# Optimization experiments

Hardware: AMD Instinct MI355X
Metric: run time of the kernel (lower is better)

## Reference

```python
import jax, jax.numpy as jnp
import numpy as np

ENTITY_ID_COL = 0  # EntityState 'id' attribute column
NUM_NPC_TYPES = 5
LN_EPS = 1e-5
NEG = -1e9


def layernorm(x, g, b):
    m = jnp.mean(x, axis=-1, keepdims=True)
    v = jnp.mean((x - m) ** 2, axis=-1, keepdims=True)
    return (x - m) * jax.lax.rsqrt(v + LN_EPS) * g + b


def gat_layer(x, mask, W, a_src, a_dst, ln_g, ln_b, num_heads, concat):
    B, N, _ = x.shape
    D = a_src.shape[-1]
    h = jnp.matmul(x, W).reshape(B, N, num_heads, D)          # [B,N,H,D]
    e_i = jnp.sum(h * a_src, axis=-1)                          # [B,N,H]
    e_j = jnp.sum(h * a_dst, axis=-1)                          # [B,N,H]
    # additive attention: e[b,i,j,h] = leakyrelu(e_i[b,i,h] + e_j[b,j,h])
    e = jax.nn.leaky_relu(e_i[:, :, None, :] + e_j[:, None, :, :], 0.2)
    mm = mask[:, :, None, None] * mask[:, None, :, None]       # [B,N,N,1]
    e = jnp.where(mm == 0, NEG, e)
    attn = jax.nn.softmax(e, axis=2)                           # softmax over j
    h_prime = jnp.einsum('bnjh,bjhd->bnhd', attn, h)
    if concat:
        h_prime = h_prime.reshape(B, N, num_heads * D)
    else:
        h_prime = h_prime.mean(axis=2)
    if h_prime.shape[-1] == x.shape[-1]:
        h_prime = layernorm(h_prime + x, ln_g, ln_b)
    else:
        h_prime = layernorm(h_prime, ln_g, ln_b)
    return h_prime


def setup_inputs() -> dict:
    key = jax.random.key(0)
    ks = jax.random.split(key, 12)
    B, N = 8, 1024
    entity_dim, hidden, heads, input_size = 31, 256, 4, 256
    d_head = hidden // heads  # 64
    merged_dim = entity_dim + 4  # 35 (npc_type expanded to 5 one-hot cols)

    agents = jax.random.normal(ks[0], (B, N, entity_dim), dtype=jnp.float32)
    npc_type = jax.random.randint(ks[1], (B, N), 0, NUM_NPC_TYPES).astype(jnp.float32)
    valid = (jax.random.uniform(ks[2], (B, N)) < 0.9).astype(jnp.float32)
    ids = jnp.arange(1, N + 1, dtype=jnp.float32)[None, :] * valid
    ids = ids.at[:, 0].set(1.0)  # guarantee id 1 exists in every batch row
    agents = agents.at[:, :, 0].set(ids)
    agents = agents.at[:, :, 1].set(npc_type)
    my_id = jnp.ones((B,), dtype=jnp.int32)

    def xavier(k, shape, fan_in, fan_out, gain=1.414):
        bound = gain * np.sqrt(6.0 / (fan_in + fan_out))
        return jax.random.uniform(k, shape, jnp.float32, -bound, bound)

    Wp = xavier(ks[3], (merged_dim, hidden), merged_dim, hidden, 1.0)
    bp = jnp.zeros((hidden,), jnp.float32)
    W1 = xavier(ks[4], (hidden, heads * d_head), hidden, heads * d_head)
    a_src1 = xavier(ks[5], (heads, d_head), heads, d_head)
    a_dst1 = xavier(ks[6], (heads, d_head), heads, d_head)
    ln1_g = jnp.ones((heads * d_head,), jnp.float32)
    ln1_b = jnp.zeros((heads * d_head,), jnp.float32)
    W2 = xavier(ks[7], (hidden, heads * d_head), hidden, heads * d_head)
    a_src2 = xavier(ks[8], (heads, d_head), heads, d_head)
    a_dst2 = xavier(ks[9], (heads, d_head), heads, d_head)
    ln2_g = jnp.ones((d_head,), jnp.float32)
    ln2_b = jnp.zeros((d_head,), jnp.float32)
    Wa = xavier(ks[10], (d_head, hidden), d_head, hidden, 1.0)
    ba = jnp.zeros((hidden,), jnp.float32)
    Wm = xavier(ks[11], (d_head, input_size), d_head, input_size, 1.0)
    bm = jnp.zeros((input_size,), jnp.float32)
    return dict(agents=agents, my_id=my_id, Wp=Wp, bp=bp,
                W1=W1, a_src1=a_src1, a_dst1=a_dst1, ln1_g=ln1_g, ln1_b=ln1_b,
                W2=W2, a_src2=a_src2, a_dst2=a_dst2, ln2_g=ln2_g, ln2_b=ln2_b,
                Wa=Wa, ba=ba, Wm=Wm, bm=bm)


def reference(agents, my_id, Wp, bp, W1, a_src1, a_dst1, ln1_g, ln1_b,
              W2, a_src2, a_dst2, ln2_g, ln2_b, Wa, ba, Wm, bm):
    num_heads = a_src1.shape[0]
    npc_type = agents[:, :, 1].astype(jnp.int32)
    one_hot = jax.nn.one_hot(npc_type, NUM_NPC_TYPES, dtype=jnp.float32)
    merged = jnp.concatenate([agents[:, :, :1], one_hot, agents[:, :, 2:]], axis=-1)
    mask = (merged[:, :, ENTITY_ID_COL] != 0).astype(jnp.float32)   # [B,N]
    proj = jnp.matmul(merged, Wp) + bp                              # [B,N,hidden]
    h1 = jax.nn.relu(gat_layer(proj, mask, W1, a_src1, a_dst1, ln1_g, ln1_b, num_heads, True))
    h2 = jax.nn.relu(gat_layer(h1, mask, W2, a_src2, a_dst2, ln2_g, ln2_b, num_heads, False))
    agent_embeddings = jnp.matmul(h2, Wa) + ba                      # [B,N,hidden]
    self_mask = merged[:, :, ENTITY_ID_COL] == my_id[:, None].astype(jnp.float32)
    idx = jnp.argmax(self_mask.astype(jnp.int32), axis=1)           # [B]
    my_emb = h2[jnp.arange(h2.shape[0]), idx]                       # [B,d_head]
    my_emb = jax.nn.relu(jnp.matmul(my_emb, Wm) + bm)
    return (agent_embeddings, my_emb)
```

## Files before the change

### kernel.cpp

```cpp
#include <hip/hip_runtime.h>
#include <hip/hip_bf16.h>

typedef _Float16 f16x8 __attribute__((ext_vector_type(8)));
typedef float f32x4 __attribute__((ext_vector_type(4)));

__global__ __launch_bounds__(256) void k_proj(
    const float* __restrict__ agents, const int* __restrict__ my_id,
    const float* __restrict__ Wp, const float* __restrict__ bp,
    float* __restrict__ proj, float* __restrict__ mask, int* __restrict__ idx)
{
  int blk = blockIdx.x;
  int b = blk >> 10, n = blk & 1023;
  __shared__ float arow[32];
  int t = threadIdx.x;
  if (t < 31) arow[t] = agents[((size_t)(b * 1024 + n)) * 31 + t];
  __syncthreads();
  float id = arow[0];
  int npc = (int)arow[1];
  float acc = bp[t] + id * Wp[t] + Wp[(1 + npc) * 256 + t];
#pragma unroll
  for (int c = 2; c < 31; ++c) acc += arow[c] * Wp[(4 + c) * 256 + t];
  proj[((size_t)(b * 1024 + n)) * 256 + t] = acc;
  if (t == 0) {
    mask[b * 1024 + n] = (id != 0.f) ? 1.f : 0.f;
    if (id == (float)my_id[b]) atomicMin(&idx[b], n);
  }
}

__global__ __launch_bounds__(256) void k_gemm(
    const float* __restrict__ A, const float* __restrict__ B,
    const float* __restrict__ bias, float* __restrict__ C, int K)
{
  __shared__ float As[64][68];
  __shared__ float Bs[64][68];
  int tid = threadIdx.x;
  int bi = blockIdx.x >> 2, bj = blockIdx.x & 3;
  int i0 = bi << 6, j0 = bj << 6;
  int ti4 = (tid & 15) << 2, tj4 = (tid >> 4) << 2;
  int r = tid >> 2, c0 = (tid & 3) << 4;
  float acc[4][4];
#pragma unroll
  for (int a = 0; a < 4; ++a)
#pragma unroll
    for (int q = 0; q < 4; ++q) acc[a][q] = 0.f;

  for (int k0 = 0; k0 < K; k0 += 64) {
    const float4* Ap4 = (const float4*)(A + (size_t)(i0 + r) * K + k0 + c0);
    float4 aa0 = Ap4[0], aa1 = Ap4[1], aa2 = Ap4[2], aa3 = Ap4[3];
    As[c0 + 0][r] = aa0.x; As[c0 + 1][r] = aa0.y; As[c0 + 2][r] = aa0.z; As[c0 + 3][r] = aa0.w;
    As[c0 + 4][r] = aa1.x; As[c0 + 5][r] = aa1.y; As[c0 + 6][r] = aa1.z; As[c0 + 7][r] = aa1.w;
    As[c0 + 8][r] = aa2.x; As[c0 + 9][r] = aa2.y; As[c0 +10][r] = aa2.z; As[c0 +11][r] = aa2.w;
    As[c0 +12][r] = aa3.x; As[c0 +13][r] = aa3.y; As[c0 +14][r] = aa3.z; As[c0 +15][r] = aa3.w;
    const float4* Bp4 = (const float4*)(B + (size_t)(k0 + r) * 256 + j0 + c0);
    float4 bb0 = Bp4[0], bb1 = Bp4[1], bb2 = Bp4[2], bb3 = Bp4[3];
    *(float4*)&Bs[r][c0 + 0]  = bb0;
    *(float4*)&Bs[r][c0 + 4]  = bb1;
    *(float4*)&Bs[r][c0 + 8]  = bb2;
    *(float4*)&Bs[r][c0 + 12] = bb3;
    __syncthreads();
#pragma unroll
    for (int k = 0; k < 64; ++k) {
      float4 av = *(const float4*)&As[k][ti4];
      float4 bv = *(const float4*)&Bs[k][tj4];
      acc[0][0] += av.x * bv.x; acc[0][1] += av.x * bv.y; acc[0][2] += av.x * bv.z; acc[0][3] += av.x * bv.w;
      acc[1][0] += av.y * bv.x; acc[1][1] += av.y * bv.y; acc[1][2] += av.y * bv.z; acc[1][3] += av.y * bv.w;
      acc[2][0] += av.z * bv.x; acc[2][1] += av.z * bv.y; acc[2][2] += av.z * bv.z; acc[2][3] += av.z * bv.w;
      acc[3][0] += av.w * bv.x; acc[3][1] += av.w * bv.y; acc[3][2] += av.w * bv.z; acc[3][3] += av.w * bv.w;
    }
    __syncthreads();
  }
  float4 bb;
  if (bias) bb = *(const float4*)&bias[j0 + tj4];
  else { bb.x = bb.y = bb.z = bb.w = 0.f; }
#pragma unroll
  for (int ii = 0; ii < 4; ++ii) {
    float4 o;
    o.x = acc[ii][0] + bb.x; o.y = acc[ii][1] + bb.y;
    o.z = acc[ii][2] + bb.z; o.w = acc[ii][3] + bb.w;
    *(float4*)&C[(size_t)(i0 + ti4 + ii) * 256 + j0 + tj4] = o;
  }
}

__global__ __launch_bounds__(256) void k_edges(
    const float* __restrict__ h, const float* __restrict__ a_src,
    const float* __restrict__ a_dst, float* __restrict__ esrc, float* __restrict__ edst)
{
  __shared__ float as_[256], ad_[256];
  int t = threadIdx.x;
  as_[t] = a_src[t];
  ad_[t] = a_dst[t];
  __syncthreads();
  int w = t >> 6, l = t & 63;
  int row = blockIdx.x * 4 + w;
  const float* x = h + (size_t)row * 256;
  float ps[4], pd[4];
#pragma unroll
  for (int hh = 0; hh < 4; ++hh) {
    float v = x[hh * 64 + l];
    ps[hh] = v * as_[hh * 64 + l];
    pd[hh] = v * ad_[hh * 64 + l];
  }
#pragma unroll
  for (int hh = 0; hh < 4; ++hh) {
    for (int o = 32; o; o >>= 1) {
      ps[hh] += __shfl_down(ps[hh], o);
      pd[hh] += __shfl_down(pd[hh], o);
    }
  }
  if (l == 0) {
    int b = row >> 10, n = row & 1023;
#pragma unroll
    for (int hh = 0; hh < 4; ++hh) {
      esrc[((b * 4 + hh) << 10) + n] = ps[hh];
      edst[((b * 4 + hh) << 10) + n] = pd[hh];
    }
  }
}

__global__ __launch_bounds__(256) void k_emax(
    const float* __restrict__ edst, const float* __restrict__ mask, float* __restrict__ Mmax)
{
  int bh = blockIdx.x;
  int b = bh >> 2;
  int t = threadIdx.x;
  float v = -1e30f;
  for (int j = t; j < 1024; j += 256)
    if (mask[(b << 10) + j] != 0.f) v = fmaxf(v, edst[(bh << 10) + j]);
  for (int o = 32; o; o >>= 1) v = fmaxf(v, __shfl_down(v, o));
  __shared__ float red[4];
  if ((t & 63) == 0) red[t >> 6] = v;
  __syncthreads();
  if (t == 0) Mmax[bh] = fmaxf(fmaxf(red[0], red[1]), fmaxf(red[2], red[3]));
}

__global__ __launch_bounds__(256) void k_prep(
    const float* __restrict__ h, _Float16* __restrict__ hT)
{
  int blk = blockIdx.x;
  int c = blk & 31, hh = (blk >> 5) & 3, b = blk >> 7;
  int t = threadIdx.x;
  __shared__ _Float16 tile[32][72];
  {
    int jr = t >> 3, dg = t & 7;
    const float* src = h + ((size_t)(b * 1024 + c * 32 + jr)) * 256 + hh * 64 + dg * 8;
    float4 a = *(const float4*)src;
    float4 b4 = *(const float4*)(src + 4);
    _Float16* tp = &tile[jr][dg * 8];
    tp[0] = (_Float16)a.x;  tp[1] = (_Float16)a.y;  tp[2] = (_Float16)a.z;  tp[3] = (_Float16)a.w;
    tp[4] = (_Float16)b4.x; tp[5] = (_Float16)b4.y; tp[6] = (_Float16)b4.z; tp[7] = (_Float16)b4.w;
  }
  __syncthreads();
  {
    int d = t >> 2, q = t & 3;
    _Float16 o[8];
#pragma unroll
    for (int s = 0; s < 8; ++s) o[s] = tile[q * 8 + s][d];
    _Float16* dst = hT + ((size_t)((b * 4 + hh) * 32 + c)) * 2048 + d * 32 + q * 8;
    *(uint4*)dst = *(const uint4*)o;
  }
}

template <int LAYER>
__global__ __launch_bounds__(256) void k_attn_mfma(
    const _Float16* __restrict__ hT, const float* __restrict__ esrc,
    const float* __restrict__ edst, const float* __restrict__ Mmax,
    const float* __restrict__ mask, const float* __restrict__ resid,
    const float* __restrict__ g, const float* __restrict__ be,
    float* __restrict__ out)
{
  __shared__ __align__(16) char smem[40960];
  __shared__ float esrcL[16][4], mL[16][4];
  __shared__ float maskL[16], MhL[4];
  __shared__ float sInvS[4][16];
  __shared__ float statM[16], statR[16];

  int t = threadIdx.x;
  int hID = t >> 6, l = t & 63;
  int b = blockIdx.x & 7;
  int it = blockIdx.x >> 3;
  int i0 = it << 4;

  if (t < 16) maskL[t] = mask[(b << 10) + i0 + t];
  if (t < 4) MhL[t] = Mmax[(b << 2) + t];
  if (t < 64) {
    int ii = t >> 2, hh = t & 3;
    esrcL[ii][hh] = esrc[(((b << 2) + hh) << 10) + i0 + ii];
  }
  __syncthreads();
  if (t < 64) {
    int ii = t >> 2, hh = t & 3;
    float m = 0.f;
    if (maskL[ii] != 0.f) {
      float v = esrcL[ii][hh] + MhL[hh];
      m = v > 0.f ? v : 0.2f * v;
    }
    mL[ii][hh] = m;
  }
  __syncthreads();

  int iloc = l & 15;
  float esr = esrcL[iloc][hID];
  float mr = mL[iloc][hID];
  float mskI = maskL[iloc];
  int jg = (l >> 4) << 3;

  const float* ej_base = edst + (((b << 2) + hID) << 10);
  const float* mk_base = mask + (b << 10);
  const char* gT = (const char*)hT + ((size_t)((b * 4 + hID) * 32)) * 4096;
  char* hb = smem + hID * 10240;

  f32x4 C0 = {0.f,0.f,0.f,0.f}, C1 = C0, C2 = C0, C3 = C0;
  float sp = 0.f;

  {
    const uint4* gs = (const uint4*)(gT + l * 64);
    uint4 s0 = gs[0], s1 = gs[1], s2 = gs[2], s3 = gs[3];
    uint4* wp = (uint4*)(hb + l * 80);
    wp[0] = s0; wp[1] = s1; wp[2] = s2; wp[3] = s3;
  }
  int cur = 0;

  for (int c = 0; c < 32; ++c) {
    uint4 n0, n1, n2, n3;
    if (c < 31) {
      const uint4* gs = (const uint4*)(gT + (size_t)(c + 1) * 4096 + l * 64);
      n0 = gs[0]; n1 = gs[1]; n2 = gs[2]; n3 = gs[3];
    }
    int j0 = c << 5;
    float4 e0 = *(const float4*)(ej_base + j0 + jg);
    float4 e1 = *(const float4*)(ej_base + j0 + jg + 4);
    float4 m0 = *(const float4*)(mk_base + j0 + jg);
    float4 m1 = *(const float4*)(mk_base + j0 + jg + 4);
    float w[8];
    float ev[8] = {e0.x, e0.y, e0.z, e0.w, e1.x, e1.y, e1.z, e1.w};
    float mv[8] = {m0.x, m0.y, m0.z, m0.w, m1.x, m1.y, m1.z, m1.w};
    if (mskI != 0.f) {
#pragma unroll
      for (int q = 0; q < 8; ++q) {
        float v = esr + ev[q];
        v = v > 0.f ? v : 0.2f * v;
        w[q] = (mv[q] != 0.f) ? __expf(v - mr) : 0.f;
      }
    } else {
#pragma unroll
      for (int q = 0; q < 8; ++q) w[q] = 1.f;
    }
    f16x8 af;
#pragma unroll
    for (int q = 0; q < 8; ++q) { sp += w[q]; af[q] = (_Float16)w[q]; }
    const char* rp = hb + cur * 5120 + (l & 15) * 80 + (l >> 4) * 16;
    f16x8 b0 = *(const f16x8*)(rp);
    f16x8 b1 = *(const f16x8*)(rp + 1280);
    f16x8 b2 = *(const f16x8*)(rp + 2560);
    f16x8 b3 = *(const f16x8*)(rp + 3840);
    C0 = __builtin_amdgcn_mfma_f32_16x16x32_f16(af, b0, C0, 0, 0, 0);
    C1 = __builtin_amdgcn_mfma_f32_16x16x32_f16(af, b1, C1, 0, 0, 0);
    C2 = __builtin_amdgcn_mfma_f32_16x16x32_f16(af, b2, C2, 0, 0, 0);
    C3 = __builtin_amdgcn_mfma_f32_16x16x32_f16(af, b3, C3, 0, 0, 0);
    if (c < 31) {
      uint4* wp = (uint4*)(hb + (cur ^ 1) * 5120 + l * 80);
      wp[0] = n0; wp[1] = n1; wp[2] = n2; wp[3] = n3;
      cur ^= 1;
    }
  }

  sp += __shfl_xor(sp, 16);
  sp += __shfl_xor(sp, 32);
  if (l < 16) sInvS[hID][l] = 1.f / sp;
  __syncthreads();

  float (*y)[256] = (float (*)[256])smem;
  {
    int rbase = (l >> 4) << 2;
    int col = (hID << 6) + (l & 15);
#pragma unroll
    for (int r = 0; r < 4; ++r) {
      float sv = sInvS[hID][rbase + r];
      y[rbase + r][col +  0] = C0[r] * sv;
      y[rbase + r][col + 16] = C1[r] * sv;
      y[rbase + r][col + 32] = C2[r] * sv;
      y[rbase + r][col + 48] = C3[r] * sv;
    }
  }
  __syncthreads();

  if (LAYER == 1) {
#pragma unroll
    for (int i = 0; i < 16; ++i)
      y[i][t] += resid[((size_t)(b * 1024 + i0 + i)) * 256 + t];
    __syncthreads();
#pragma unroll
    for (int rr = 0; rr < 4; ++rr) {
      int i = (hID << 2) + rr;
      float v0 = y[i][l], v1 = y[i][64 + l], v2 = y[i][128 + l], v3 = y[i][192 + l];
      float s = v0 + v1 + v2 + v3;
      float q = v0 * v0 + v1 * v1 + v2 * v2 + v3 * v3;
      for (int o = 32; o; o >>= 1) { s += __shfl_xor(s, o); q += __shfl_xor(q, o); }
      if (l == 0) {
        float mean = s * (1.f / 256.f);
        float var = q * (1.f / 256.f) - mean * mean;
        statM[i] = mean;
        statR[i] = rsqrtf(var + 1e-5f);
      }
    }
    __syncthreads();
#pragma unroll
    for (int i = 0; i < 16; ++i) {
      float yv = y[i][t];
      float o_ = (yv - statM[i]) * statR[i] * g[t] + be[t];
      out[((size_t)(b * 1024 + i0 + i)) * 256 + t] = fmaxf(o_, 0.f);
    }
  } else {
#pragma unroll
    for (int rr = 0; rr < 4; ++rr) {
      int i = (hID << 2) + rr;
      float v = 0.25f * (y[i][l] + y[i][64 + l] + y[i][128 + l] + y[i][192 + l]);
      float s = v, q = v * v;
      for (int o = 32; o; o >>= 1) { s += __shfl_xor(s, o); q += __shfl_xor(q, o); }
      float mean = s * (1.f / 64.f);
      float var = q * (1.f / 64.f) - mean * mean;
      float rstd = rsqrtf(var + 1e-5f);
      float o_ = (v - mean) * rstd * g[l] + be[l];
      out[((size_t)(b * 1024 + i0 + i)) * 64 + l] = fmaxf(o_, 0.f);
    }
  }
}

__global__ __launch_bounds__(256) void k_myemb(
    const float* __restrict__ h2, const int* __restrict__ idx,
    const float* __restrict__ Wm, const float* __restrict__ bm, float* __restrict__ out)
{
  __shared__ float row[64];
  int t = threadIdx.x;
  for (int b = 0; b < 8; ++b) {
    int n = idx[b];
    if (t < 64) row[t] = h2[((size_t)(b * 1024 + n)) * 64 + t];
    __syncthreads();
    float acc = bm[t];
#pragma unroll
    for (int d = 0; d < 64; ++d) acc += row[d] * Wm[d * 256 + t];
    out[2097152 + b * 256 + t] = fmaxf(acc, 0.f);
    __syncthreads();
  }
}

extern "C" void kernel_launch(void* const* d_in, const int* in_sizes, int n_in,
                              void* d_out, int out_size, void* d_ws, size_t ws_size,
                              hipStream_t stream) {
  const float* agents = (const float*)d_in[0];
  const int* my_id = (const int*)d_in[1];
  const float* Wp = (const float*)d_in[2];
  const float* bp = (const float*)d_in[3];
  const float* W1 = (const float*)d_in[4];
  const float* a_src1 = (const float*)d_in[5];
  const float* a_dst1 = (const float*)d_in[6];
  const float* ln1_g = (const float*)d_in[7];
  const float* ln1_b = (const float*)d_in[8];
  const float* W2 = (const float*)d_in[9];
  const float* a_src2 = (const float*)d_in[10];
  const float* a_dst2 = (const float*)d_in[11];
  const float* ln2_g = (const float*)d_in[12];
  const float* ln2_b = (const float*)d_in[13];
  const float* Wa = (const float*)d_in[14];
  const float* ba = (const float*)d_in[15];
  const float* Wm = (const float*)d_in[16];
  const float* bm = (const float*)d_in[17];
  float* out = (float*)d_out;

  float* W = (float*)d_ws;
  float* mask = W;
  float* Mmax = W + 8192;
  int* idx = (int*)(W + 8224);
  float* esrc = W + 16384;
  float* edst = W + 49152;
  float* proj = W + 81920;
  float* htmp = W + 2179072;
  float* h1 = W + 4276224;
  float* h2 = W + 6373376;
  _Float16* hT = (_Float16*)(W + 6897664);

  hipMemsetAsync(idx, 0x7F, 8 * sizeof(int), stream);
  k_proj<<<8192, 256, 0, stream>>>(agents, my_id, Wp, bp, proj, mask, idx);

  k_gemm<<<512, 256, 0, stream>>>(proj, W1, nullptr, htmp, 256);
  k_prep<<<1024, 256, 0, stream>>>(htmp, hT);
  k_edges<<<2048, 256, 0, stream>>>(htmp, a_src1, a_dst1, esrc, edst);
  k_emax<<<32, 256, 0, stream>>>(edst, mask, Mmax);
  k_attn_mfma<1><<<512, 256, 0, stream>>>(hT, esrc, edst, Mmax, mask, proj, ln1_g, ln1_b, h1);

  k_gemm<<<512, 256, 0, stream>>>(h1, W2, nullptr, htmp, 256);
  k_prep<<<1024, 256, 0, stream>>>(htmp, hT);
  k_edges<<<2048, 256, 0, stream>>>(htmp, a_src2, a_dst2, esrc, edst);
  k_emax<<<32, 256, 0, stream>>>(edst, mask, Mmax);
  k_attn_mfma<2><<<512, 256, 0, stream>>>(hT, esrc, edst, Mmax, mask, nullptr, ln2_g, ln2_b, h2);

  k_gemm<<<512, 256, 0, stream>>>(h2, Wa, ba, out, 64);
  k_myemb<<<1, 256, 0, stream>>>(h2, idx, Wm, bm, out);
}
```

Measured before the change: 243.1 us.

## Replace FP32 SIMT GEMMs with split-fp16 MFMA GEMMs using pre-transposed weights

Swaps the scalar FP32 tiled GEMM for an MFMA 16x16x32 f16 kernel. Each fp32 operand is split into hi and lo halves, and three MFMAs per tile keep accuracy close to fp32. Weights are transposed each call by a small k_wt kernel so B tiles load contiguously along K. This trades scalar FMA throughput for matrix-core throughput, at the cost of extra conversion work, three extra launches, and more syncs per K step with a smaller 32-wide K tile.

Measured after the change: 235.8 us. 1.03x faster.

```diff
diff --git a/kernel.cpp b/kernel.cpp
--- a/kernel.cpp
+++ b/kernel.cpp
@@ -27,57 +27,116 @@
   }
 }
 
-__global__ __launch_bounds__(256) void k_gemm(
-    const float* __restrict__ A, const float* __restrict__ B,
-    const float* __restrict__ bias, float* __restrict__ C, int K)
-{
-  __shared__ float As[64][68];
-  __shared__ float Bs[64][68];
-  int tid = threadIdx.x;
+__global__ __launch_bounds__(256) void k_wt(
+    const float* __restrict__ W, float* __restrict__ Wt, int K)
+{
+  __shared__ float tl[32][33];
+  int bk = blockIdx.x >> 3, bj = blockIdx.x & 7;
+  int tc = threadIdx.x & 31, tr = threadIdx.x >> 5;
+#pragma unroll
+  for (int r = 0; r < 4; ++r) {
+    int row = tr * 4 + r;
+    tl[row][tc] = W[(size_t)(bk * 32 + row) * 256 + bj * 32 + tc];
+  }
+  __syncthreads();
+#pragma unroll
+  for (int r = 0; r < 4; ++r) {
+    int row = tr * 4 + r;
+    Wt[(size_t)(bj * 32 + row) * K + bk * 32 + tc] = tl[tc][row];
+  }
+}
+
+template <int K>
+__global__ __launch_bounds__(256) void k_gemm_mfma(
+    const float* __restrict__ A, const float* __restrict__ BtF,
+    const float* __restrict__ bias, float* __restrict__ C)
+{
+  __shared__ __align__(16) _Float16 AsH[64 * 40], AsL[64 * 40];
+  __shared__ __align__(16) _Float16 BsH[64 * 40], BsL[64 * 40];
+  int t = threadIdx.x;
+  int w = t >> 6, l = t & 63;
   int bi = blockIdx.x >> 2, bj = blockIdx.x & 3;
   int i0 = bi << 6, j0 = bj << 6;
-  int ti4 = (tid & 15) << 2, tj4 = (tid >> 4) << 2;
-  int r = tid >> 2, c0 = (tid & 3) << 4;
-  float acc[4][4];
-#pragma unroll
-  for (int a = 0; a < 4; ++a)
-#pragma unroll
-    for (int q = 0; q < 4; ++q) acc[a][q] = 0.f;
-
-  for (int k0 = 0; k0 < K; k0 += 64) {
-    const float4* Ap4 = (const float4*)(A + (size_t)(i0 + r) * K + k0 + c0);
-    float4 aa0 = Ap4[0], aa1 = Ap4[1], aa2 = Ap4[2], aa3 = Ap4[3];
-    As[c0 + 0][r] = aa0.x; As[c0 + 1][r] = aa0.y; As[c0 + 2][r] = aa0.z; As[c0 + 3][r] = aa0.w;
-    As[c0 + 4][r] = aa1.x; As[c0 + 5][r] = aa1.y; As[c0 + 6][r] = aa1.z; As[c0 + 7][r] = aa1.w;
-    As[c0 + 8][r] = aa2.x; As[c0 + 9][r] = aa2.y; As[c0 +10][r] = aa2.z; As[c0 +11][r] = aa2.w;
-    As[c0 +12][r] = aa3.x; As[c0 +13][r] = aa3.y; As[c0 +14][r] = aa3.z; As[c0 +15][r] = aa3.w;
-    const float4* Bp4 = (const float4*)(B + (size_t)(k0 + r) * 256 + j0 + c0);
-    float4 bb0 = Bp4[0], bb1 = Bp4[1], bb2 = Bp4[2], bb3 = Bp4[3];
-    *(float4*)&Bs[r][c0 + 0]  = bb0;
-    *(float4*)&Bs[r][c0 + 4]  = bb1;
-    *(float4*)&Bs[r][c0 + 8]  = bb2;
-    *(float4*)&Bs[r][c0 + 12] = bb3;
-    __syncthreads();
-#pragma unroll
-    for (int k = 0; k < 64; ++k) {
-      float4 av = *(const float4*)&As[k][ti4];
-      float4 bv = *(const float4*)&Bs[k][tj4];
-      acc[0][0] += av.x * bv.x; acc[0][1] += av.x * bv.y; acc[0][2] += av.x * bv.z; acc[0][3] += av.x * bv.w;
-      acc[1][0] += av.y * bv.x; acc[1][1] += av.y * bv.y; acc[1][2] += av.y * bv.z; acc[1][3] += av.y * bv.w;
-      acc[2][0] += av.z * bv.x; acc[2][1] += av.z * bv.y; acc[2][2] += av.z * bv.z; acc[2][3] += av.z * bv.w;
-      acc[3][0] += av.w * bv.x; acc[3][1] += av.w * bv.y; acc[3][2] += av.w * bv.z; acc[3][3] += av.w * bv.w;
-    }
-    __syncthreads();
-  }
-  float4 bb;
-  if (bias) bb = *(const float4*)&bias[j0 + tj4];
-  else { bb.x = bb.y = bb.z = bb.w = 0.f; }
-#pragma unroll
-  for (int ii = 0; ii < 4; ++ii) {
-    float4 o;
-    o.x = acc[ii][0] + bb.x; o.y = acc[ii][1] + bb.y;
-    o.z = acc[ii][2] + bb.z; o.w = acc[ii][3] + bb.w;
-    *(float4*)&C[(size_t)(i0 + ti4 + ii) * 256 + j0 + tj4] = o;
+  int srow = t >> 2, skq = (t & 3) << 3;
+
+  f32x4 C0 = {0.f, 0.f, 0.f, 0.f}, C1 = C0, C2 = C0, C3 = C0;
+
+  for (int k0 = 0; k0 < K; k0 += 32) {
+    {
+      const float* ap = A + (size_t)(i0 + srow) * K + k0 + skq;
+      float4 a0 = *(const float4*)ap, a1 = *(const float4*)(ap + 4);
+      float av[8] = {a0.x, a0.y, a0.z, a0.w, a1.x, a1.y, a1.z, a1.w};
+      _Float16 hi[8], lo[8];
+#pragma unroll
+      for (int q = 0; q < 8; ++q) {
+        hi[q] = (_Float16)av[q];
+        lo[q] = (_Float16)(av[q] - (float)hi[q]);
+      }
+      *(uint4*)&AsH[srow * 40 + skq] = *(const uint4*)hi;
+      *(uint4*)&AsL[srow * 40 + skq] = *(const uint4*)lo;
+    }
+    {
+      const float* bp = BtF + (size_t)(j0 + srow) * K + k0 + skq;
+      float4 b0 = *(const float4*)bp, b1 = *(const float4*)(bp + 4);
+      float bv[8] = {b0.x, b0.y, b0.z, b0.w, b1.x, b1.y, b1.z, b1.w};
+      _Float16 hi[8], lo[8];
+#pragma unroll
+      for (int q = 0; q < 8; ++q) {
+        hi[q] = (_Float16)bv[q];
+        lo[q] = (_Float16)(bv[q] - (float)hi[q]);
+      }
+      *(uint4*)&BsH[srow * 40 + skq] = *(const uint4*)hi;
+      *(uint4*)&BsL[srow * 40 + skq] = *(const uint4*)lo;
+    }
+    __syncthreads();
+    int fr = l & 15;
+    int fk = (l >> 4) << 3;
+    f16x8 ah = *(const f16x8*)&AsH[(w * 16 + fr) * 40 + fk];
+    f16x8 al = *(const f16x8*)&AsL[(w * 16 + fr) * 40 + fk];
+    {
+      f16x8 bh = *(const f16x8*)&BsH[(0 * 16 + fr) * 40 + fk];
+      f16x8 bl = *(const f16x8*)&BsL[(0 * 16 + fr) * 40 + fk];
+      C0 = __builtin_amdgcn_mfma_f32_16x16x32_f16(ah, bh, C0, 0, 0, 0);
+      C0 = __builtin_amdgcn_mfma_f32_16x16x32_f16(ah, bl, C0, 0, 0, 0);
+      C0 = __builtin_amdgcn_mfma_f32_16x16x32_f16(al, bh, C0, 0, 0, 0);
+    }
+    {
+      f16x8 bh = *(const f16x8*)&BsH[(1 * 16 + fr) * 40 + fk];
+      f16x8 bl = *(const f16x8*)&BsL[(1 * 16 + fr) * 40 + fk];
+      C1 = __builtin_amdgcn_mfma_f32_16x16x32_f16(ah, bh, C1, 0, 0, 0);
+      C1 = __builtin_amdgcn_mfma_f32_16x16x32_f16(ah, bl, C1, 0, 0, 0);
+      C1 = __builtin_amdgcn_mfma_f32_16x16x32_f16(al, bh, C1, 0, 0, 0);
+    }
+    {
+      f16x8 bh = *(const f16x8*)&BsH[(2 * 16 + fr) * 40 + fk];
+      f16x8 bl = *(const f16x8*)&BsL[(2 * 16 + fr) * 40 + fk];
+      C2 = __builtin_amdgcn_mfma_f32_16x16x32_f16(ah, bh, C2, 0, 0, 0);
+      C2 = __builtin_amdgcn_mfma_f32_16x16x32_f16(ah, bl, C2, 0, 0, 0);
+      C2 = __builtin_amdgcn_mfma_f32_16x16x32_f16(al, bh, C2, 0, 0, 0);
+    }
+    {
+      f16x8 bh = *(const f16x8*)&BsH[(3 * 16 + fr) * 40 + fk];
+      f16x8 bl = *(const f16x8*)&BsL[(3 * 16 + fr) * 40 + fk];
+      C3 = __builtin_amdgcn_mfma_f32_16x16x32_f16(ah, bh, C3, 0, 0, 0);
+      C3 = __builtin_amdgcn_mfma_f32_16x16x32_f16(ah, bl, C3, 0, 0, 0);
+      C3 = __builtin_amdgcn_mfma_f32_16x16x32_f16(al, bh, C3, 0, 0, 0);
+    }
+    __syncthreads();
+  }
+
+  int rbase = i0 + w * 16 + ((l >> 4) << 2);
+  int cb = j0 + (l & 15);
+  float b0 = bias ? bias[cb] : 0.f;
+  float b1 = bias ? bias[cb + 16] : 0.f;
+  float b2 = bias ? bias[cb + 32] : 0.f;
+  float b3 = bias ? bias[cb + 48] : 0.f;
+#pragma unroll
+  for (int r = 0; r < 4; ++r) {
+    size_t ro = (size_t)(rbase + r) * 256;
+    C[ro + cb]      = C0[r] + b0;
+    C[ro + cb + 16] = C1[r] + b1;
+    C[ro + cb + 32] = C2[r] + b2;
+    C[ro + cb + 48] = C3[r] + b3;
   }
 }
 
@@ -378,22 +437,28 @@
   float* h1 = W + 4276224;
   float* h2 = W + 6373376;
   _Float16* hT = (_Float16*)(W + 6897664);
+  float* Wt1 = W + 7946240;
+  float* Wt2 = W + 8011776;
+  float* Wta = W + 8077312;
 
   hipMemsetAsync(idx, 0x7F, 8 * sizeof(int), stream);
   k_proj<<<8192, 256, 0, stream>>>(agents, my_id, Wp, bp, proj, mask, idx);
-
-  k_gemm<<<512, 256, 0, stream>>>(proj, W1, nullptr, htmp, 256);
+  k_wt<<<64, 256, 0, stream>>>(W1, Wt1, 256);
+  k_wt<<<64, 256, 0, stream>>>(W2, Wt2, 256);
+  k_wt<<<16, 256, 0, stream>>>(Wa, Wta, 64);
+
+  k_gemm_mfma<256><<<512, 256, 0, stream>>>(proj, Wt1, nullptr, htmp);
   k_prep<<<1024, 256, 0, stream>>>(htmp, hT);
   k_edges<<<2048, 256, 0, stream>>>(htmp, a_src1, a_dst1, esrc, edst);
   k_emax<<<32, 256, 0, stream>>>(edst, mask, Mmax);
   k_attn_mfma<1><<<512, 256, 0, stream>>>(hT, esrc, edst, Mmax, mask, proj, ln1_g, ln1_b, h1);
 
-  k_gemm<<<512, 256, 0, stream>>>(h1, W2, nullptr, htmp, 256);
+  k_gemm_mfma<256><<<512, 256, 0, stream>>>(h1, Wt2, nullptr, htmp);
   k_prep<<<1024, 256, 0, stream>>>(htmp, hT);
   k_edges<<<2048, 256, 0, stream>>>(htmp, a_src2, a_dst2, esrc, edst);
   k_emax<<<32, 256, 0, stream>>>(edst, mask, Mmax);
   k_attn_mfma<2><<<512, 256, 0, stream>>>(hT, esrc, edst, Mmax, mask, nullptr, ln2_g, ln2_b, h2);
 
-  k_gemm<<<512, 256, 0, stream>>>(h2, Wa, ba, out, 64);
+  k_gemm_mfma<64><<<512, 256, 0, stream>>>(h2, Wta, ba, out);
   k_myemb<<<1, 256, 0, stream>>>(h2, idx, Wm, bm, out);
 }
```
